# Optimization experiments

Hardware: AMD Instinct MI355X
Metric: run time of the kernel (lower is better)

Reference implementation:

```python
import jax, jax.numpy as jnp
import numpy as np

B, S, I, H = 32, 512, 512, 512


def _complex_tanh(r, i):
    mag = jnp.maximum(jnp.sqrt(r * r + i * i + 1e-14), 1e-8)
    t = jnp.tanh(mag)
    return t * (r / mag), t * (i / mag)


def setup_inputs() -> dict:
    key = jax.random.key(0)
    ks = jax.random.split(key, 32)
    stdv = 1.0 / np.sqrt(H)
    def u(k, shape):
        return jax.random.uniform(k, shape, jnp.float32, -stdv, stdv)
    inp = {
        "z_real": jax.random.normal(ks[0], (B, S, I), jnp.float32),
        "z_imag": jax.random.normal(ks[1], (B, S, I), jnp.float32),
    }
    idx = 2
    for g in ["i", "f", "c", "o"]:
        inp[f"W_z{g}_real"] = u(ks[idx], (I, H)); idx += 1
        inp[f"W_z{g}_imag"] = u(ks[idx], (I, H)); idx += 1
        inp[f"W_h{g}_real"] = u(ks[idx], (H, H)); idx += 1
        inp[f"W_h{g}_imag"] = u(ks[idx], (H, H)); idx += 1
        inp[f"b_{g}_real"] = u(ks[idx], (H,)); idx += 1
        inp[f"b_{g}_imag"] = u(ks[idx], (H,)); idx += 1
    return inp


def reference(z_real, z_imag,
              W_zi_real, W_zi_imag, W_hi_real, W_hi_imag, b_i_real, b_i_imag,
              W_zf_real, W_zf_imag, W_hf_real, W_hf_imag, b_f_real, b_f_imag,
              W_zc_real, W_zc_imag, W_hc_real, W_hc_imag, b_c_real, b_c_imag,
              W_zo_real, W_zo_imag, W_ho_real, W_ho_imag, b_o_real, b_o_imag):
    # Precompute input-side contributions for all timesteps in one batched GEMM each.
    def xproj(Wr, Wi, br):  # real part of z @ (Wr + j Wi), plus real bias
        return (jnp.einsum('bsi,ih->bsh', z_real, Wr)
                - jnp.einsum('bsi,ih->bsh', z_imag, Wi) + br)
    xi = xproj(W_zi_real, W_zi_imag, b_i_real)
    xf = xproj(W_zf_real, W_zf_imag, b_f_real)
    xo = xproj(W_zo_real, W_zo_imag, b_o_real)
    xc_r = xproj(W_zc_real, W_zc_imag, b_c_real)
    xc_i = (jnp.einsum('bsi,ih->bsh', z_imag, W_zc_real)
            + jnp.einsum('bsi,ih->bsh', z_real, W_zc_imag) + b_c_imag)

    bsz = z_real.shape[0]
    hdim = W_hi_real.shape[0]
    init = (jnp.zeros((bsz, hdim), z_real.dtype),) * 4  # h_r, h_i, c_r, c_i

    def step(carry, x):
        h_r, h_i, c_r, c_i = carry
        xi_t, xf_t, xo_t, xcr_t, xci_t = x
        i_t = jax.nn.sigmoid(xi_t + h_r @ W_hi_real - h_i @ W_hi_imag)
        f_t = jax.nn.sigmoid(xf_t + h_r @ W_hf_real - h_i @ W_hf_imag)
        o_t = jax.nn.sigmoid(xo_t + h_r @ W_ho_real - h_i @ W_ho_imag)
        ct_r = xcr_t + h_r @ W_hc_real - h_i @ W_hc_imag
        ct_i = xci_t + h_i @ W_hc_real + h_r @ W_hc_imag
        ct_r, ct_i = _complex_tanh(ct_r, ct_i)
        c_r = f_t * c_r + i_t * ct_r
        c_i = f_t * c_i + i_t * ct_i
        th_r, th_i = _complex_tanh(c_r, c_i)
        h_r = o_t * th_r
        h_i = o_t * th_i
        return (h_r, h_i, c_r, c_i), (h_r, h_i)

    xs = tuple(a.transpose(1, 0, 2) for a in (xi, xf, xo, xc_r, xc_i))  # (S,B,H)
    (hf_r, hf_i, cf_r, cf_i), (seq_r, seq_i) = jax.lax.scan(step, init, xs)
    hseq_r = seq_r.transpose(1, 0, 2)  # (B,S,H)
    hseq_i = seq_i.transpose(1, 0, 2)
    return ((hseq_r, hseq_i), ((hf_r, hf_i), (cf_r, cf_i)))
```

## Files before the change

kernel.cpp:

```cpp
#include <hip/hip_runtime.h>

#define OFF_WZT   0ull
#define OFF_WHT   5242880ull
#define OFF_BIAS  10485760ull
#define OFF_XPERM 10496000ull
#define OFF_HBUF  94382080ull
#define NWG 256

typedef __attribute__((ext_vector_type(8))) short short8;
typedef __attribute__((ext_vector_type(4))) float f32x4;

__device__ __forceinline__ unsigned short f2bf(float f) {
  unsigned int u = __float_as_uint(f);
  u += 0x7fffu + ((u >> 16) & 1u);
  return (unsigned short)(u >> 16);
}
__device__ __forceinline__ float bf2f(unsigned short h) {
  return __uint_as_float(((unsigned int)h) << 16);
}

struct PackArgs {
  const float* zlo[5]; const float* zhi[5];
  const float* hlo[5]; const float* hhi[5];
  const float* bias[5];
};

__global__ void pack_kernel(PackArgs args, unsigned short* __restrict__ WzT,
                            unsigned short* __restrict__ WhT,
                            float* __restrict__ bias_out,
                            unsigned long long* __restrict__ Hbuf64) {
  const long long total = 2ll * 2621440ll;
  long long stride = (long long)gridDim.x * blockDim.x;
  for (long long gid = (long long)blockIdx.x * blockDim.x + threadIdx.x; gid < total; gid += stride) {
    int sel = (int)(gid >= 2621440ll);
    int e = (int)(gid - (long long)sel * 2621440ll);
    int c = e >> 10, k = e & 1023;
    int g = c >> 9, h = c & 511;
    float v;
    if (sel) {
      int kk = k >> 1, ri = k & 1;
      const float* src = ri ? args.hhi[g] : args.hlo[g];
      float sgn = (!ri || g == 4) ? 1.f : -1.f;
      v = sgn * src[kk * 512 + h];
    } else {
      int kk = k & 511;
      const float* src = (k < 512) ? args.zlo[g] : args.zhi[g];
      float sgn = (k < 512 || g == 4) ? 1.f : -1.f;
      v = sgn * src[kk * 512 + h];
    }
    (sel ? WhT : WzT)[(long long)c * 1024 + k] = f2bf(v);
  }
  int gid0 = blockIdx.x * blockDim.x + threadIdx.x;
  if (gid0 < 2560) { int g = gid0 >> 9; bias_out[gid0] = args.bias[g][gid0 & 511]; }
  if (gid0 < 32768) Hbuf64[gid0] = 0ull;
}

__global__ __launch_bounds__(256) void phase1_kernel(
    const float* __restrict__ zr, const float* __restrict__ zi,
    const unsigned short* __restrict__ WzT, const float* __restrict__ bias,
    unsigned short* __restrict__ Xperm) {
  __shared__ unsigned short Al[64 * 40];
  __shared__ unsigned short Bl[64 * 40];
  int bid = blockIdx.x;
  int bm = bid / 40, bn = bid % 40;
  int tid = threadIdx.x;
  int wave = tid >> 6, lane = tid & 63;
  int mq = wave >> 1, nq = wave & 1;
  int lr = lane & 15, lkb = (lane >> 4) * 8;
  int srow = tid >> 2, sq = tid & 3;

  f32x4 acc[2][2];
#pragma unroll
  for (int i0 = 0; i0 < 2; i0++)
#pragma unroll
    for (int j0 = 0; j0 < 2; j0++) acc[i0][j0] = (f32x4){0.f, 0.f, 0.f, 0.f};

  for (int kb = 0; kb < 32; kb++) {
    int gk = kb * 32 + sq * 8;
    const float* srcp = (gk < 512) ? (zr + (long long)(bm * 64 + srow) * 512 + gk)
                                   : (zi + (long long)(bm * 64 + srow) * 512 + (gk - 512));
    float4 f0 = *(const float4*)srcp;
    float4 f1 = *(const float4*)(srcp + 4);
    uint4 p;
    p.x = (unsigned)f2bf(f0.x) | ((unsigned)f2bf(f0.y) << 16);
    p.y = (unsigned)f2bf(f0.z) | ((unsigned)f2bf(f0.w) << 16);
    p.z = (unsigned)f2bf(f1.x) | ((unsigned)f2bf(f1.y) << 16);
    p.w = (unsigned)f2bf(f1.z) | ((unsigned)f2bf(f1.w) << 16);
    *(uint4*)(&Al[srow * 40 + sq * 8]) = p;
    const unsigned short* bsrc = WzT + (long long)(bn * 64 + srow) * 1024 + kb * 32 + sq * 8;
    *(uint4*)(&Bl[srow * 40 + sq * 8]) = *(const uint4*)bsrc;
    __syncthreads();
    short8 a0 = *(const short8*)(&Al[(mq * 32 + 0 + lr) * 40 + lkb]);
    short8 a1 = *(const short8*)(&Al[(mq * 32 + 16 + lr) * 40 + lkb]);
    short8 b0 = *(const short8*)(&Bl[(nq * 32 + 0 + lr) * 40 + lkb]);
    short8 b1 = *(const short8*)(&Bl[(nq * 32 + 16 + lr) * 40 + lkb]);
    acc[0][0] = __builtin_amdgcn_mfma_f32_16x16x32_bf16(a0, b0, acc[0][0], 0, 0, 0);
    acc[0][1] = __builtin_amdgcn_mfma_f32_16x16x32_bf16(a0, b1, acc[0][1], 0, 0, 0);
    acc[1][0] = __builtin_amdgcn_mfma_f32_16x16x32_bf16(a1, b0, acc[1][0], 0, 0, 0);
    acc[1][1] = __builtin_amdgcn_mfma_f32_16x16x32_bf16(a1, b1, acc[1][1], 0, 0, 0);
    __syncthreads();
  }
#pragma unroll
  for (int mt = 0; mt < 2; mt++)
#pragma unroll
    for (int nt = 0; nt < 2; nt++) {
      int C = bn * 64 + nq * 32 + nt * 16 + lr;
      float bv = bias[C];
      int g = C >> 9, h = C & 511;
      int wgc = h >> 3, jj = h & 7;
#pragma unroll
      for (int r = 0; r < 4; r++) {
        int R = bm * 64 + mq * 32 + mt * 16 + (lane >> 4) * 4 + r;
        int bb = R >> 9, tt = R & 511;
        float v = acc[mt][nt][r] + bv;
        Xperm[(((long long)(tt * 64 + wgc)) * 32 + bb) * 40 + g * 8 + jj] = f2bf(v);
      }
    }
}

__global__ __launch_bounds__(384) void recur_kernel(
    const unsigned short* __restrict__ WhT,
    const unsigned short* __restrict__ Xperm,
    unsigned long long* __restrict__ Hbuf64,
    float* __restrict__ out) {
  extern __shared__ unsigned short lds[];
  unsigned short* Wl = lds;
  unsigned int* Hl32 = (unsigned int*)(lds + 41280);
  float* gates = (float*)((char*)(lds + 41280) + 32768);

  int bid = blockIdx.x;
  int d = bid >> 6, wl = bid & 63;
  int tid = threadIdx.x;
  int wave = tid >> 6, lane = tid & 63;
  int nt = wave % 3, kh = wave / 3;
  int lr = lane & 15, kq = lane >> 4;

  for (int idx = tid; idx < 5120; idx += 384) {
    int r = idx >> 7, ch = idx & 127;
    int gcol = (r >> 3) * 512 + wl * 8 + (r & 7);
    uint4 v = *(const uint4*)(WhT + (long long)gcol * 1024 + ch * 8);
    *(uint4*)(&Wl[r * 1032 + ch * 8]) = v;
  }
  {
    uint4 z = {0u, 0u, 0u, 0u};
    for (int idx = tid; idx < 2048; idx += 384) ((uint4*)Hl32)[idx] = z;
  }
  __syncthreads();

  unsigned long long* Hme = Hbuf64 + d * 8192;
  const int nch = (tid < 256) ? 11 : 10;
  const unsigned need = (tid < 256) ? 0x7FFu : 0x3FFu;

  float c_r = 0.f, c_i = 0.f;
  int er = tid >> 3, ej = tid & 7;

  for (int t = 0; t < 512; t++) {
    float xg[5];
    if (tid < 64) {
      const unsigned short* xp = Xperm + (((long long)(t * 64 + wl)) * 32 + (8 * d + er)) * 40;
#pragma unroll
      for (int g = 0; g < 5; g++) xg[g] = bf2f(xp[g * 8 + ej]);
    }

    if (t > 0) {
      const unsigned long long* hb = Hme + ((t - 1) & 1) * 4096;
      unsigned long long v[11];
      unsigned got = 0;
      while (true) {
#pragma unroll
        for (int p = 0; p < 11; p++) {
          if (p < nch && !(got & (1u << p)))
            v[p] = __hip_atomic_load(hb + tid + p * 384, __ATOMIC_RELAXED,
                                     __HIP_MEMORY_SCOPE_AGENT);
        }
        unsigned g2 = got;
#pragma unroll
        for (int p = 0; p < 11; p++)
          if (p < nch && !(got & (1u << p)) && (unsigned)(v[p] >> 32) == (unsigned)t)
            g2 |= 1u << p;
        got = g2;
        if (got == need) break;
        __builtin_amdgcn_s_sleep(1);
      }
#pragma unroll
      for (int p = 0; p < 11; p++)
        if (p < nch) {
          int c = tid + p * 384;
          Hl32[((c >> 5) * 16 + ((c >> 2) & 7)) * 4 + (c & 3)] = (unsigned)v[p];
        }
    }
    __syncthreads();

    f32x4 acc0 = {0.f, 0.f, 0.f, 0.f};
    f32x4 acc1 = {0.f, 0.f, 0.f, 0.f};
    const unsigned short* Hls = (const unsigned short*)Hl32;
#pragma unroll
    for (int kk = 0; kk < 8; kk++) {
      int ka = kh * 16 + kk;
      short8 a = *(const short8*)(Hls + (ka * 4 + kq) * 128 + lr * 8);
      short8 b = *(const short8*)(&Wl[(nt * 16 + lr) * 1032 + ka * 32 + kq * 8]);
      acc0 = __builtin_amdgcn_mfma_f32_16x16x32_bf16(a, b, acc0, 0, 0, 0);
    }
#pragma unroll
    for (int kk = 8; kk < 16; kk++) {
      int ka = kh * 16 + kk;
      short8 a = *(const short8*)(Hls + (ka * 4 + kq) * 128 + lr * 8);
      short8 b = *(const short8*)(&Wl[(nt * 16 + lr) * 1032 + ka * 32 + kq * 8]);
      acc1 = __builtin_amdgcn_mfma_f32_16x16x32_bf16(a, b, acc1, 0, 0, 0);
    }
    {
      int r0 = (lane >> 4) * 4;
#pragma unroll
      for (int r = 0; r < 4; r++)
        gates[wave * 256 + (r0 + r) * 16 + lr] = acc0[r] + acc1[r];
    }
    __syncthreads();

    if (tid < 64) {
      float gv[5];
#pragma unroll
      for (int g = 0; g < 5; g++) {
        int c = g * 8 + ej, tn = c >> 4, cw = c & 15;
        gv[g] = gates[tn * 256 + er * 16 + cw] + gates[(3 + tn) * 256 + er * 16 + cw] + xg[g];
      }
      float ig = 1.f / (1.f + __expf(-gv[0]));
      float fg = 1.f / (1.f + __expf(-gv[1]));
      float og = 1.f / (1.f + __expf(-gv[2]));
      float crp = gv[3], cip = gv[4];
      float mag = fmaxf(sqrtf(crp * crp + cip * cip + 1e-14f), 1e-8f);
      float e1 = __expf(-2.f * mag);
      float s1 = ((1.f - e1) / (1.f + e1)) / mag;
      c_r = fg * c_r + ig * (crp * s1);
      c_i = fg * c_i + ig * (cip * s1);
      float mag2 = fmaxf(sqrtf(c_r * c_r + c_i * c_i + 1e-14f), 1e-8f);
      float e2 = __expf(-2.f * mag2);
      float s2 = ((1.f - e2) / (1.f + e2)) / mag2;
      float hr = og * (c_r * s2);
      float hi = og * (c_i * s2);
      int j = wl * 8 + ej;
      int cidx = ((j >> 2) * 8 + er) * 4 + (j & 3);
      unsigned hv = (unsigned)f2bf(hr) | ((unsigned)f2bf(hi) << 16);
      __hip_atomic_store(Hme + (t & 1) * 4096 + cidx,
                         ((unsigned long long)(t + 1) << 32) | hv,
                         __ATOMIC_RELAXED, __HIP_MEMORY_SCOPE_AGENT);
      int b = 8 * d + er;
      out[(long long)b * 262144 + t * 512 + j] = hr;
      out[8388608ll + (long long)b * 262144 + t * 512 + j] = hi;
      if (t == 511) {
        out[16777216ll + b * 512 + j] = hr;
        out[16793600ll + b * 512 + j] = hi;
        out[16809984ll + b * 512 + j] = c_r;
        out[16826368ll + b * 512 + j] = c_i;
      }
    }
  }
}

extern "C" void kernel_launch(void* const* d_in, const int* in_sizes, int n_in,
                              void* d_out, int out_size, void* d_ws, size_t ws_size,
                              hipStream_t stream) {
  const float* zr = (const float*)d_in[0];
  const float* zi = (const float*)d_in[1];
  const int gi = 2, gf = 8, gc = 14, go = 20;
  PackArgs pa;
  const int gbase[5] = {gi, gf, go, gc, gc};
  for (int g = 0; g < 5; g++) {
    int b = gbase[g];
    if (g < 4) {
      pa.zlo[g] = (const float*)d_in[b + 0];
      pa.zhi[g] = (const float*)d_in[b + 1];
      pa.hlo[g] = (const float*)d_in[b + 2];
      pa.hhi[g] = (const float*)d_in[b + 3];
    } else {
      pa.zlo[g] = (const float*)d_in[b + 1];
      pa.zhi[g] = (const float*)d_in[b + 0];
      pa.hlo[g] = (const float*)d_in[b + 3];
      pa.hhi[g] = (const float*)d_in[b + 2];
    }
  }
  pa.bias[0] = (const float*)d_in[gi + 4];
  pa.bias[1] = (const float*)d_in[gf + 4];
  pa.bias[2] = (const float*)d_in[go + 4];
  pa.bias[3] = (const float*)d_in[gc + 4];
  pa.bias[4] = (const float*)d_in[gc + 5];

  char* ws = (char*)d_ws;
  unsigned short* WzT = (unsigned short*)(ws + OFF_WZT);
  unsigned short* WhT = (unsigned short*)(ws + OFF_WHT);
  float* bias = (float*)(ws + OFF_BIAS);
  unsigned short* Xperm = (unsigned short*)(ws + OFF_XPERM);
  unsigned long long* Hbuf64 = (unsigned long long*)(ws + OFF_HBUF);

  pack_kernel<<<2048, 256, 0, stream>>>(pa, WzT, WhT, bias, Hbuf64);
  phase1_kernel<<<10240, 256, 0, stream>>>(zr, zi, WzT, bias, Xperm);

  const int ldsBytes = 82560 + 32768 + 6144;
  (void)hipFuncSetAttribute((const void*)recur_kernel,
                            hipFuncAttributeMaxDynamicSharedMemorySize, ldsBytes);
  recur_kernel<<<NWG, 384, ldsBytes, stream>>>(WhT, Xperm, Hbuf64, (float*)d_out);
}
```

Before: 1.771 ms.

## Keep recurrent weight fragments in registers and offload polling from gate waves

Each wave now loads its 16 B-operand fragments of the recurrent weights into registers once, staged through a reused LDS buffer in two halves. This removes the per-step LDS reads of the weights and cuts LDS use to about 41 KB. Polling for the previous step's hidden state is moved off the first wave, which computes gates, onto the other 320 threads, so the gate wave does not spin. The tanh divisions become reciprocal multiplies. In exchange the kernel holds many more VGPRs, and the remaining waves poll more entries each.

```diff
diff --git a/kernel.cpp b/kernel.cpp
--- a/kernel.cpp
+++ b/kernel.cpp
@@ -124,9 +124,9 @@
     unsigned long long* __restrict__ Hbuf64,
     float* __restrict__ out) {
   extern __shared__ unsigned short lds[];
-  unsigned short* Wl = lds;
-  unsigned int* Hl32 = (unsigned int*)(lds + 41280);
-  float* gates = (float*)((char*)(lds + 41280) + 32768);
+  unsigned short* Wlh = lds;
+  unsigned int* Hl32 = (unsigned int*)lds;
+  float* gates = (float*)((char*)lds + 32768);
 
   int bid = blockIdx.x;
   int d = bid >> 6, wl = bid & 63;
@@ -135,21 +135,39 @@
   int nt = wave % 3, kh = wave / 3;
   int lr = lane & 15, kq = lane >> 4;
 
-  for (int idx = tid; idx < 5120; idx += 384) {
-    int r = idx >> 7, ch = idx & 127;
-    int gcol = (r >> 3) * 512 + wl * 8 + (r & 7);
-    uint4 v = *(const uint4*)(WhT + (long long)gcol * 1024 + ch * 8);
-    *(uint4*)(&Wl[r * 1032 + ch * 8]) = v;
+  short8 breg[16];
+  for (int h = 0; h < 2; h++) {
+#pragma unroll
+    for (int it = 0; it < 7; it++) {
+      int idx = tid + it * 384;
+      if (idx < 2560) {
+        int r = idx >> 6, k8 = idx & 63;
+        int gcol = (r >> 3) * 512 + wl * 8 + (r & 7);
+        *(uint4*)(&Wlh[r * 520 + k8 * 8]) =
+            *(const uint4*)(WhT + (long long)gcol * 1024 + h * 512 + k8 * 8);
+      }
+    }
+    __syncthreads();
+    if (kh == h) {
+#pragma unroll
+      for (int kk = 0; kk < 16; kk++)
+        breg[kk] = *(const short8*)(&Wlh[(nt * 16 + lr) * 520 + kk * 32 + kq * 8]);
+    }
+    __syncthreads();
   }
   {
     uint4 z = {0u, 0u, 0u, 0u};
-    for (int idx = tid; idx < 2048; idx += 384) ((uint4*)Hl32)[idx] = z;
-  }
-  __syncthreads();
+#pragma unroll
+    for (int it = 0; it < 6; it++) {
+      int idx = tid + it * 384;
+      if (idx < 2048) ((uint4*)Hl32)[idx] = z;
+    }
+  }
 
   unsigned long long* Hme = Hbuf64 + d * 8192;
-  const int nch = (tid < 256) ? 11 : 10;
-  const unsigned need = (tid < 256) ? 0x7FFu : 0x3FFu;
+  int pt = tid - 64;
+  const int nch = (pt < 0) ? 0 : (pt < 256 ? 13 : 12);
+  const unsigned need = (pt < 0) ? 0u : (pt < 256 ? 0x1FFFu : 0xFFFu);
 
   float c_r = 0.f, c_i = 0.f;
   int er = tid >> 3, ej = tid & 7;
@@ -162,20 +180,19 @@
       for (int g = 0; g < 5; g++) xg[g] = bf2f(xp[g * 8 + ej]);
     }
 
-    if (t > 0) {
+    if (t > 0 && tid >= 64) {
       const unsigned long long* hb = Hme + ((t - 1) & 1) * 4096;
-      unsigned long long v[11];
+      unsigned long long v[13];
       unsigned got = 0;
       while (true) {
 #pragma unroll
-        for (int p = 0; p < 11; p++) {
+        for (int p = 0; p < 13; p++)
           if (p < nch && !(got & (1u << p)))
-            v[p] = __hip_atomic_load(hb + tid + p * 384, __ATOMIC_RELAXED,
+            v[p] = __hip_atomic_load(hb + pt + p * 320, __ATOMIC_RELAXED,
                                      __HIP_MEMORY_SCOPE_AGENT);
-        }
         unsigned g2 = got;
 #pragma unroll
-        for (int p = 0; p < 11; p++)
+        for (int p = 0; p < 13; p++)
           if (p < nch && !(got & (1u << p)) && (unsigned)(v[p] >> 32) == (unsigned)t)
             g2 |= 1u << p;
         got = g2;
@@ -183,9 +200,9 @@
         __builtin_amdgcn_s_sleep(1);
       }
 #pragma unroll
-      for (int p = 0; p < 11; p++)
+      for (int p = 0; p < 13; p++)
         if (p < nch) {
-          int c = tid + p * 384;
+          int c = pt + p * 320;
           Hl32[((c >> 5) * 16 + ((c >> 2) & 7)) * 4 + (c & 3)] = (unsigned)v[p];
         }
     }
@@ -198,15 +215,13 @@
     for (int kk = 0; kk < 8; kk++) {
       int ka = kh * 16 + kk;
       short8 a = *(const short8*)(Hls + (ka * 4 + kq) * 128 + lr * 8);
-      short8 b = *(const short8*)(&Wl[(nt * 16 + lr) * 1032 + ka * 32 + kq * 8]);
-      acc0 = __builtin_amdgcn_mfma_f32_16x16x32_bf16(a, b, acc0, 0, 0, 0);
+      acc0 = __builtin_amdgcn_mfma_f32_16x16x32_bf16(a, breg[kk], acc0, 0, 0, 0);
     }
 #pragma unroll
     for (int kk = 8; kk < 16; kk++) {
       int ka = kh * 16 + kk;
       short8 a = *(const short8*)(Hls + (ka * 4 + kq) * 128 + lr * 8);
-      short8 b = *(const short8*)(&Wl[(nt * 16 + lr) * 1032 + ka * 32 + kq * 8]);
-      acc1 = __builtin_amdgcn_mfma_f32_16x16x32_bf16(a, b, acc1, 0, 0, 0);
+      acc1 = __builtin_amdgcn_mfma_f32_16x16x32_bf16(a, breg[kk], acc1, 0, 0, 0);
     }
     {
       int r0 = (lane >> 4) * 4;
@@ -229,12 +244,12 @@
       float crp = gv[3], cip = gv[4];
       float mag = fmaxf(sqrtf(crp * crp + cip * cip + 1e-14f), 1e-8f);
       float e1 = __expf(-2.f * mag);
-      float s1 = ((1.f - e1) / (1.f + e1)) / mag;
+      float s1 = (1.f - e1) * __frcp_rn((1.f + e1) * mag);
       c_r = fg * c_r + ig * (crp * s1);
       c_i = fg * c_i + ig * (cip * s1);
       float mag2 = fmaxf(sqrtf(c_r * c_r + c_i * c_i + 1e-14f), 1e-8f);
       float e2 = __expf(-2.f * mag2);
-      float s2 = ((1.f - e2) / (1.f + e2)) / mag2;
+      float s2 = (1.f - e2) * __frcp_rn((1.f + e2) * mag2);
       float hr = og * (c_r * s2);
       float hi = og * (c_i * s2);
       int j = wl * 8 + ej;
@@ -294,7 +309,7 @@
   pack_kernel<<<2048, 256, 0, stream>>>(pa, WzT, WhT, bias, Hbuf64);
   phase1_kernel<<<10240, 256, 0, stream>>>(zr, zi, WzT, bias, Xperm);
 
-  const int ldsBytes = 82560 + 32768 + 6144;
+  const int ldsBytes = 41600;
   (void)hipFuncSetAttribute((const void*)recur_kernel,
                             hipFuncAttributeMaxDynamicSharedMemorySize, ldsBytes);
   recur_kernel<<<NWG, 384, ldsBytes, stream>>>(WhT, Xperm, Hbuf64, (float*)d_out);
```

New measurement: 1.797 ms. Within noise of the previous version (+1.4%).

## Hold recurrent weights in registers and split polling and compute waves

Applied to the files above, without the earlier changes.

The recurrent kernel now keeps each compute wave's slice of the hidden-to-hidden weights in registers, so the per-step weight reads from LDS go away. Four waves run the MFMA loop and the gate math, while four separate waves poll the global h buffer and scatter h into LDS. This leaves one barrier per timestep instead of two. The input-projection layout is reordered so each lane reads its five gate values contiguously, and the tanh divides are replaced with a reciprocal. The risk is high register pressure from 32 short8 weight registers under launch bounds of (512, 2), which could cause spills.

```diff
diff --git a/kernel.cpp b/kernel.cpp
--- a/kernel.cpp
+++ b/kernel.cpp
@@ -113,145 +113,137 @@
         int R = bm * 64 + mq * 32 + mt * 16 + (lane >> 4) * 4 + r;
         int bb = R >> 9, tt = R & 511;
         float v = acc[mt][nt][r] + bv;
-        Xperm[(((long long)(tt * 64 + wgc)) * 32 + bb) * 40 + g * 8 + jj] = f2bf(v);
-      }
-    }
-}
-
-__global__ __launch_bounds__(384) void recur_kernel(
+        Xperm[(((long long)(tt * 64 + wgc)) * 32 + bb) * 40 + jj * 5 + g] = f2bf(v);
+      }
+    }
+}
+
+__global__ __launch_bounds__(512, 2) void recur_kernel(
     const unsigned short* __restrict__ WhT,
     const unsigned short* __restrict__ Xperm,
     unsigned long long* __restrict__ Hbuf64,
     float* __restrict__ out) {
-  extern __shared__ unsigned short lds[];
-  unsigned short* Wl = lds;
-  unsigned int* Hl32 = (unsigned int*)(lds + 41280);
-  float* gates = (float*)((char*)(lds + 41280) + 32768);
+  extern __shared__ char ldsraw[];
+  unsigned int* Hl32 = (unsigned int*)ldsraw;
+  float* gatesLds = (float*)(ldsraw + 32768);
 
   int bid = blockIdx.x;
   int d = bid >> 6, wl = bid & 63;
   int tid = threadIdx.x;
   int wave = tid >> 6, lane = tid & 63;
-  int nt = wave % 3, kh = wave / 3;
   int lr = lane & 15, kq = lane >> 4;
-
-  for (int idx = tid; idx < 5120; idx += 384) {
-    int r = idx >> 7, ch = idx & 127;
-    int gcol = (r >> 3) * 512 + wl * 8 + (r & 7);
-    uint4 v = *(const uint4*)(WhT + (long long)gcol * 1024 + ch * 8);
-    *(uint4*)(&Wl[r * 1032 + ch * 8]) = v;
+  int nt = wave;
+
+  short8 breg[32];
+  if (wave < 4) {
+    int g = lr % 5;
+    int hj2 = (lr >= 5) ? 1 : 0;
+    int gcol = g * 512 + wl * 8 + nt * 2 + hj2;
+    const unsigned short* wsrc = WhT + (long long)gcol * 1024 + kq * 8;
+#pragma unroll
+    for (int kk = 0; kk < 32; kk++)
+      breg[kk] = *(const short8*)(wsrc + kk * 32);
   }
   {
     uint4 z = {0u, 0u, 0u, 0u};
-    for (int idx = tid; idx < 2048; idx += 384) ((uint4*)Hl32)[idx] = z;
-  }
-  __syncthreads();
+#pragma unroll
+    for (int i = 0; i < 4; i++) ((uint4*)Hl32)[tid + i * 512] = z;
+  }
 
   unsigned long long* Hme = Hbuf64 + d * 8192;
-  const int nch = (tid < 256) ? 11 : 10;
-  const unsigned need = (tid < 256) ? 0x7FFu : 0x3FFu;
-
   float c_r = 0.f, c_i = 0.f;
-  int er = tid >> 3, ej = tid & 7;
+  int hj = lane >> 3, r = lane & 7;
+  int pt = tid - 256;
 
   for (int t = 0; t < 512; t++) {
-    float xg[5];
-    if (tid < 64) {
-      const unsigned short* xp = Xperm + (((long long)(t * 64 + wl)) * 32 + (8 * d + er)) * 40;
-#pragma unroll
-      for (int g = 0; g < 5; g++) xg[g] = bf2f(xp[g * 8 + ej]);
-    }
-
-    if (t > 0) {
-      const unsigned long long* hb = Hme + ((t - 1) & 1) * 4096;
-      unsigned long long v[11];
-      unsigned got = 0;
-      while (true) {
-#pragma unroll
-        for (int p = 0; p < 11; p++) {
-          if (p < nch && !(got & (1u << p)))
-            v[p] = __hip_atomic_load(hb + tid + p * 384, __ATOMIC_RELAXED,
-                                     __HIP_MEMORY_SCOPE_AGENT);
+    if (wave < 4) {
+      float xg[5];
+      if (lane < 16) {
+        const unsigned short* xp =
+            Xperm + (((long long)(t * 64 + wl)) * 32 + (8 * d + r)) * 40 + (nt * 2 + hj) * 5;
+#pragma unroll
+        for (int g = 0; g < 5; g++) xg[g] = bf2f(xp[g]);
+      }
+      __syncthreads();
+
+      f32x4 acc[4];
+#pragma unroll
+      for (int q = 0; q < 4; q++) acc[q] = (f32x4){0.f, 0.f, 0.f, 0.f};
+      const unsigned short* Hls = (const unsigned short*)Hl32;
+#pragma unroll
+      for (int kk = 0; kk < 32; kk++) {
+        short8 a = *(const short8*)(Hls + (kk * 4 + kq) * 128 + lr * 8);
+        acc[kk & 3] = __builtin_amdgcn_mfma_f32_16x16x32_bf16(a, breg[kk], acc[kk & 3], 0, 0, 0);
+      }
+      f32x4 as = (acc[0] + acc[1]) + (acc[2] + acc[3]);
+
+      float* gb = gatesLds + wave * 256;
+#pragma unroll
+      for (int q = 0; q < 4; q++) gb[q * 64 + lane] = as[q];
+
+      if (lane < 16) {
+        int q = lane & 3, s = (lane & 7) >> 2;
+        float gv[5];
+#pragma unroll
+        for (int g = 0; g < 5; g++)
+          gv[g] = gb[q * 64 + (hj * 5 + g + 16 * s)] + xg[g];
+        float ig = 1.f / (1.f + __expf(-gv[0]));
+        float fg = 1.f / (1.f + __expf(-gv[1]));
+        float og = 1.f / (1.f + __expf(-gv[2]));
+        float crp = gv[3], cip = gv[4];
+        float mag = fmaxf(sqrtf(crp * crp + cip * cip + 1e-14f), 1e-8f);
+        float e1 = __expf(-2.f * mag);
+        float s1 = (1.f - e1) * __frcp_rn((1.f + e1) * mag);
+        c_r = fg * c_r + ig * (crp * s1);
+        c_i = fg * c_i + ig * (cip * s1);
+        float mag2 = fmaxf(sqrtf(c_r * c_r + c_i * c_i + 1e-14f), 1e-8f);
+        float e2 = __expf(-2.f * mag2);
+        float s2 = (1.f - e2) * __frcp_rn((1.f + e2) * mag2);
+        float hr = og * (c_r * s2);
+        float hi = og * (c_i * s2);
+        int j = wl * 8 + nt * 2 + hj;
+        int cidx = ((j >> 2) * 8 + r) * 4 + (j & 3);
+        unsigned hv = (unsigned)f2bf(hr) | ((unsigned)f2bf(hi) << 16);
+        __hip_atomic_store(Hme + (t & 1) * 4096 + cidx,
+                           ((unsigned long long)(t + 1) << 32) | hv,
+                           __ATOMIC_RELAXED, __HIP_MEMORY_SCOPE_AGENT);
+        int b = 8 * d + r;
+        out[(long long)b * 262144 + t * 512 + j] = hr;
+        out[8388608ll + (long long)b * 262144 + t * 512 + j] = hi;
+        if (t == 511) {
+          out[16777216ll + b * 512 + j] = hr;
+          out[16793600ll + b * 512 + j] = hi;
+          out[16809984ll + b * 512 + j] = c_r;
+          out[16826368ll + b * 512 + j] = c_i;
         }
-        unsigned g2 = got;
-#pragma unroll
-        for (int p = 0; p < 11; p++)
-          if (p < nch && !(got & (1u << p)) && (unsigned)(v[p] >> 32) == (unsigned)t)
-            g2 |= 1u << p;
-        got = g2;
-        if (got == need) break;
-        __builtin_amdgcn_s_sleep(1);
-      }
-#pragma unroll
-      for (int p = 0; p < 11; p++)
-        if (p < nch) {
-          int c = tid + p * 384;
+      }
+    } else {
+      if (t > 0) {
+        const unsigned long long* hb = Hme + ((t - 1) & 1) * 4096;
+        unsigned long long v[16];
+        unsigned got = 0;
+        while (true) {
+#pragma unroll
+          for (int p = 0; p < 16; p++)
+            if (!(got & (1u << p)))
+              v[p] = __hip_atomic_load(hb + pt + p * 256, __ATOMIC_RELAXED,
+                                       __HIP_MEMORY_SCOPE_AGENT);
+          unsigned g2 = got;
+#pragma unroll
+          for (int p = 0; p < 16; p++)
+            if (!(got & (1u << p)) && (unsigned)(v[p] >> 32) == (unsigned)t)
+              g2 |= 1u << p;
+          got = g2;
+          if (got == 0xFFFFu) break;
+          __builtin_amdgcn_s_sleep(1);
+        }
+#pragma unroll
+        for (int p = 0; p < 16; p++) {
+          int c = pt + p * 256;
           Hl32[((c >> 5) * 16 + ((c >> 2) & 7)) * 4 + (c & 3)] = (unsigned)v[p];
         }
-    }
-    __syncthreads();
-
-    f32x4 acc0 = {0.f, 0.f, 0.f, 0.f};
-    f32x4 acc1 = {0.f, 0.f, 0.f, 0.f};
-    const unsigned short* Hls = (const unsigned short*)Hl32;
-#pragma unroll
-    for (int kk = 0; kk < 8; kk++) {
-      int ka = kh * 16 + kk;
-      short8 a = *(const short8*)(Hls + (ka * 4 + kq) * 128 + lr * 8);
-      short8 b = *(const short8*)(&Wl[(nt * 16 + lr) * 1032 + ka * 32 + kq * 8]);
-      acc0 = __builtin_amdgcn_mfma_f32_16x16x32_bf16(a, b, acc0, 0, 0, 0);
-    }
-#pragma unroll
-    for (int kk = 8; kk < 16; kk++) {
-      int ka = kh * 16 + kk;
-      short8 a = *(const short8*)(Hls + (ka * 4 + kq) * 128 + lr * 8);
-      short8 b = *(const short8*)(&Wl[(nt * 16 + lr) * 1032 + ka * 32 + kq * 8]);
-      acc1 = __builtin_amdgcn_mfma_f32_16x16x32_bf16(a, b, acc1, 0, 0, 0);
-    }
-    {
-      int r0 = (lane >> 4) * 4;
-#pragma unroll
-      for (int r = 0; r < 4; r++)
-        gates[wave * 256 + (r0 + r) * 16 + lr] = acc0[r] + acc1[r];
-    }
-    __syncthreads();
-
-    if (tid < 64) {
-      float gv[5];
-#pragma unroll
-      for (int g = 0; g < 5; g++) {
-        int c = g * 8 + ej, tn = c >> 4, cw = c & 15;
-        gv[g] = gates[tn * 256 + er * 16 + cw] + gates[(3 + tn) * 256 + er * 16 + cw] + xg[g];
-      }
-      float ig = 1.f / (1.f + __expf(-gv[0]));
-      float fg = 1.f / (1.f + __expf(-gv[1]));
-      float og = 1.f / (1.f + __expf(-gv[2]));
-      float crp = gv[3], cip = gv[4];
-      float mag = fmaxf(sqrtf(crp * crp + cip * cip + 1e-14f), 1e-8f);
-      float e1 = __expf(-2.f * mag);
-      float s1 = ((1.f - e1) / (1.f + e1)) / mag;
-      c_r = fg * c_r + ig * (crp * s1);
-      c_i = fg * c_i + ig * (cip * s1);
-      float mag2 = fmaxf(sqrtf(c_r * c_r + c_i * c_i + 1e-14f), 1e-8f);
-      float e2 = __expf(-2.f * mag2);
-      float s2 = ((1.f - e2) / (1.f + e2)) / mag2;
-      float hr = og * (c_r * s2);
-      float hi = og * (c_i * s2);
-      int j = wl * 8 + ej;
-      int cidx = ((j >> 2) * 8 + er) * 4 + (j & 3);
-      unsigned hv = (unsigned)f2bf(hr) | ((unsigned)f2bf(hi) << 16);
-      __hip_atomic_store(Hme + (t & 1) * 4096 + cidx,
-                         ((unsigned long long)(t + 1) << 32) | hv,
-                         __ATOMIC_RELAXED, __HIP_MEMORY_SCOPE_AGENT);
-      int b = 8 * d + er;
-      out[(long long)b * 262144 + t * 512 + j] = hr;
-      out[8388608ll + (long long)b * 262144 + t * 512 + j] = hi;
-      if (t == 511) {
-        out[16777216ll + b * 512 + j] = hr;
-        out[16793600ll + b * 512 + j] = hi;
-        out[16809984ll + b * 512 + j] = c_r;
-        out[16826368ll + b * 512 + j] = c_i;
-      }
+      }
+      __syncthreads();
     }
   }
 }
@@ -294,8 +286,8 @@
   pack_kernel<<<2048, 256, 0, stream>>>(pa, WzT, WhT, bias, Hbuf64);
   phase1_kernel<<<10240, 256, 0, stream>>>(zr, zi, WzT, bias, Xperm);
 
-  const int ldsBytes = 82560 + 32768 + 6144;
+  const int ldsBytes = 81920;
   (void)hipFuncSetAttribute((const void*)recur_kernel,
                             hipFuncAttributeMaxDynamicSharedMemorySize, ldsBytes);
-  recur_kernel<<<NWG, 384, ldsBytes, stream>>>(WhT, Xperm, Hbuf64, (float*)d_out);
-}
+  recur_kernel<<<NWG, 512, ldsBytes, stream>>>(WhT, Xperm, Hbuf64, (float*)d_out);
+}
```

Result: slower. 2.001 ms (+13.0%).

## Split recurrence across 512 workgroups with register-resident weights and sentinel sync

Applied to the files above, without the earlier changes.

The recurrent kernel now runs 512 workgroups, each handling 4 batch rows instead of 8, so the per-step cross-workgroup exchange per group is smaller. The recurrent weight slice moves from LDS into registers, and LDS shrinks to a small H buffer plus the gate scratch. Each workgroup spins on a per-group sentinel array before reading the tagged H values. The design depends on all 512 workgroups being co-resident for the spin barrier, and it wastes MFMA lanes because only 4 of the 16 A rows are used.

```diff
diff --git a/kernel.cpp b/kernel.cpp
--- a/kernel.cpp
+++ b/kernel.cpp
@@ -5,7 +5,8 @@
 #define OFF_BIAS  10485760ull
 #define OFF_XPERM 10496000ull
 #define OFF_HBUF  94382080ull
-#define NWG 256
+#define OFF_SENT  94644224ull
+#define NWG 512
 
 typedef __attribute__((ext_vector_type(8))) short short8;
 typedef __attribute__((ext_vector_type(4))) float f32x4;
@@ -28,7 +29,8 @@
 __global__ void pack_kernel(PackArgs args, unsigned short* __restrict__ WzT,
                             unsigned short* __restrict__ WhT,
                             float* __restrict__ bias_out,
-                            unsigned long long* __restrict__ Hbuf64) {
+                            unsigned long long* __restrict__ Hbuf64,
+                            unsigned int* __restrict__ Sent) {
   const long long total = 2ll * 2621440ll;
   long long stride = (long long)gridDim.x * blockDim.x;
   for (long long gid = (long long)blockIdx.x * blockDim.x + threadIdx.x; gid < total; gid += stride) {
@@ -53,6 +55,7 @@
   int gid0 = blockIdx.x * blockDim.x + threadIdx.x;
   if (gid0 < 2560) { int g = gid0 >> 9; bias_out[gid0] = args.bias[g][gid0 & 511]; }
   if (gid0 < 32768) Hbuf64[gid0] = 0ull;
+  if (gid0 < 512) Sent[gid0] = 0u;
 }
 
 __global__ __launch_bounds__(256) void phase1_kernel(
@@ -118,15 +121,14 @@
     }
 }
 
-__global__ __launch_bounds__(384) void recur_kernel(
+__global__ __launch_bounds__(384, 3) void recur_kernel(
     const unsigned short* __restrict__ WhT,
     const unsigned short* __restrict__ Xperm,
     unsigned long long* __restrict__ Hbuf64,
+    unsigned int* __restrict__ Sent,
     float* __restrict__ out) {
-  extern __shared__ unsigned short lds[];
-  unsigned short* Wl = lds;
-  unsigned int* Hl32 = (unsigned int*)(lds + 41280);
-  float* gates = (float*)((char*)(lds + 41280) + 32768);
+  __shared__ unsigned int Hl32[2048 + 16];
+  __shared__ float gates[1536];
 
   int bid = blockIdx.x;
   int d = bid >> 6, wl = bid & 63;
@@ -135,122 +137,132 @@
   int nt = wave % 3, kh = wave / 3;
   int lr = lane & 15, kq = lane >> 4;
 
-  for (int idx = tid; idx < 5120; idx += 384) {
-    int r = idx >> 7, ch = idx & 127;
-    int gcol = (r >> 3) * 512 + wl * 8 + (r & 7);
-    uint4 v = *(const uint4*)(WhT + (long long)gcol * 1024 + ch * 8);
-    *(uint4*)(&Wl[r * 1032 + ch * 8]) = v;
-  }
+  short8 breg[16];
   {
-    uint4 z = {0u, 0u, 0u, 0u};
-    for (int idx = tid; idx < 2048; idx += 384) ((uint4*)Hl32)[idx] = z;
-  }
+    int c = nt * 16 + lr; if (c > 39) c = 39;
+    int g = c >> 3, jj = c & 7;
+    int gcol = g * 512 + wl * 8 + jj;
+    const unsigned short* wsrc = WhT + (long long)gcol * 1024 + kh * 512 + kq * 8;
+#pragma unroll
+    for (int kk = 0; kk < 16; kk++)
+      breg[kk] = *(const short8*)(wsrc + kk * 32);
+  }
+  for (int i = tid; i < 2064; i += 384) Hl32[i] = 0u;
   __syncthreads();
 
-  unsigned long long* Hme = Hbuf64 + d * 8192;
-  const int nch = (tid < 256) ? 11 : 10;
-  const unsigned need = (tid < 256) ? 0x7FFu : 0x3FFu;
-
+  unsigned long long* Hme = Hbuf64 + d * 4096;
+  unsigned int* Sme = Sent + d * 64;
   float c_r = 0.f, c_i = 0.f;
-  int er = tid >> 3, ej = tid & 7;
+  int er = lane >> 3, ej = lane & 7;
+  int np = (tid < 128) ? 6 : 5;
 
   for (int t = 0; t < 512; t++) {
     float xg[5];
-    if (tid < 64) {
-      const unsigned short* xp = Xperm + (((long long)(t * 64 + wl)) * 32 + (8 * d + er)) * 40;
+    if (wave == 0 && lane < 32) {
+      const unsigned short* xp =
+          Xperm + (((long long)(t * 64 + wl)) * 32 + (4 * d + er)) * 40;
 #pragma unroll
       for (int g = 0; g < 5; g++) xg[g] = bf2f(xp[g * 8 + ej]);
     }
 
     if (t > 0) {
-      const unsigned long long* hb = Hme + ((t - 1) & 1) * 4096;
-      unsigned long long v[11];
-      unsigned got = 0;
       while (true) {
-#pragma unroll
-        for (int p = 0; p < 11; p++) {
-          if (p < nch && !(got & (1u << p)))
+        unsigned sv = __hip_atomic_load(Sme + lane, __ATOMIC_RELAXED,
+                                        __HIP_MEMORY_SCOPE_AGENT);
+        if (__all(sv >= (unsigned)t)) break;
+        __builtin_amdgcn_s_sleep(1);
+      }
+      const unsigned long long* hb = Hme + ((t - 1) & 1) * 2048;
+      unsigned long long v[6];
+#pragma unroll
+      for (int p = 0; p < 6; p++)
+        if (p < np)
+          v[p] = __hip_atomic_load(hb + tid + p * 384, __ATOMIC_RELAXED,
+                                   __HIP_MEMORY_SCOPE_AGENT);
+#pragma unroll
+      for (int p = 0; p < 6; p++)
+        if (p < np) {
+          while ((unsigned)(v[p] >> 32) != (unsigned)t)
             v[p] = __hip_atomic_load(hb + tid + p * 384, __ATOMIC_RELAXED,
                                      __HIP_MEMORY_SCOPE_AGENT);
-        }
-        unsigned g2 = got;
-#pragma unroll
-        for (int p = 0; p < 11; p++)
-          if (p < nch && !(got & (1u << p)) && (unsigned)(v[p] >> 32) == (unsigned)t)
-            g2 |= 1u << p;
-        got = g2;
-        if (got == need) break;
-        __builtin_amdgcn_s_sleep(1);
-      }
-#pragma unroll
-      for (int p = 0; p < 11; p++)
-        if (p < nch) {
-          int c = tid + p * 384;
-          Hl32[((c >> 5) * 16 + ((c >> 2) & 7)) * 4 + (c & 3)] = (unsigned)v[p];
+          Hl32[tid + p * 384] = (unsigned)v[p];
         }
     }
     __syncthreads();
 
     f32x4 acc0 = {0.f, 0.f, 0.f, 0.f};
     f32x4 acc1 = {0.f, 0.f, 0.f, 0.f};
-    const unsigned short* Hls = (const unsigned short*)Hl32;
 #pragma unroll
     for (int kk = 0; kk < 8; kk++) {
       int ka = kh * 16 + kk;
-      short8 a = *(const short8*)(Hls + (ka * 4 + kq) * 128 + lr * 8);
-      short8 b = *(const short8*)(&Wl[(nt * 16 + lr) * 1032 + ka * 32 + kq * 8]);
-      acc0 = __builtin_amdgcn_mfma_f32_16x16x32_bf16(a, b, acc0, 0, 0, 0);
+      const unsigned int* ap = (lr < 4) ? (Hl32 + ((ka * 4 + kq) * 4 + lr) * 4)
+                                        : (Hl32 + 2048);
+      short8 a = *(const short8*)ap;
+      acc0 = __builtin_amdgcn_mfma_f32_16x16x32_bf16(a, breg[kk], acc0, 0, 0, 0);
     }
 #pragma unroll
     for (int kk = 8; kk < 16; kk++) {
       int ka = kh * 16 + kk;
-      short8 a = *(const short8*)(Hls + (ka * 4 + kq) * 128 + lr * 8);
-      short8 b = *(const short8*)(&Wl[(nt * 16 + lr) * 1032 + ka * 32 + kq * 8]);
-      acc1 = __builtin_amdgcn_mfma_f32_16x16x32_bf16(a, b, acc1, 0, 0, 0);
+      const unsigned int* ap = (lr < 4) ? (Hl32 + ((ka * 4 + kq) * 4 + lr) * 4)
+                                        : (Hl32 + 2048);
+      short8 a = *(const short8*)ap;
+      acc1 = __builtin_amdgcn_mfma_f32_16x16x32_bf16(a, breg[kk], acc1, 0, 0, 0);
     }
     {
-      int r0 = (lane >> 4) * 4;
+      f32x4 as = acc0 + acc1;
+      int r0 = kq * 4;
 #pragma unroll
       for (int r = 0; r < 4; r++)
-        gates[wave * 256 + (r0 + r) * 16 + lr] = acc0[r] + acc1[r];
+        gates[wave * 256 + (r0 + r) * 16 + lr] = as[r];
     }
     __syncthreads();
 
-    if (tid < 64) {
-      float gv[5];
-#pragma unroll
-      for (int g = 0; g < 5; g++) {
-        int c = g * 8 + ej, tn = c >> 4, cw = c & 15;
-        gv[g] = gates[tn * 256 + er * 16 + cw] + gates[(3 + tn) * 256 + er * 16 + cw] + xg[g];
+    if (wave == 0) {
+      float hr = 0.f, hi = 0.f;
+      if (lane < 32) {
+        float gv[5];
+#pragma unroll
+        for (int g = 0; g < 5; g++) {
+          int c = g * 8 + ej, tn = c >> 4, cw = c & 15;
+          gv[g] = gates[tn * 256 + er * 16 + cw] +
+                  gates[(3 + tn) * 256 + er * 16 + cw] + xg[g];
+        }
+        float ig = 1.f / (1.f + __expf(-gv[0]));
+        float fg = 1.f / (1.f + __expf(-gv[1]));
+        float og = 1.f / (1.f + __expf(-gv[2]));
+        float crp = gv[3], cip = gv[4];
+        float mag = fmaxf(sqrtf(crp * crp + cip * cip + 1e-14f), 1e-8f);
+        float e1 = __expf(-2.f * mag);
+        float s1 = (1.f - e1) * __frcp_rn((1.f + e1) * mag);
+        c_r = fg * c_r + ig * (crp * s1);
+        c_i = fg * c_i + ig * (cip * s1);
+        float mag2 = fmaxf(sqrtf(c_r * c_r + c_i * c_i + 1e-14f), 1e-8f);
+        float e2 = __expf(-2.f * mag2);
+        float s2 = (1.f - e2) * __frcp_rn((1.f + e2) * mag2);
+        hr = og * (c_r * s2);
+        hi = og * (c_i * s2);
+        int j = wl * 8 + ej;
+        int ci = (j >> 2) * 16 + er * 4 + (j & 3);
+        unsigned hv = (unsigned)f2bf(hr) | ((unsigned)f2bf(hi) << 16);
+        __hip_atomic_store(Hme + (t & 1) * 2048 + ci,
+                           ((unsigned long long)(t + 1) << 32) | hv,
+                           __ATOMIC_RELAXED, __HIP_MEMORY_SCOPE_AGENT);
       }
-      float ig = 1.f / (1.f + __expf(-gv[0]));
-      float fg = 1.f / (1.f + __expf(-gv[1]));
-      float og = 1.f / (1.f + __expf(-gv[2]));
-      float crp = gv[3], cip = gv[4];
-      float mag = fmaxf(sqrtf(crp * crp + cip * cip + 1e-14f), 1e-8f);
-      float e1 = __expf(-2.f * mag);
-      float s1 = ((1.f - e1) / (1.f + e1)) / mag;
-      c_r = fg * c_r + ig * (crp * s1);
-      c_i = fg * c_i + ig * (cip * s1);
-      float mag2 = fmaxf(sqrtf(c_r * c_r + c_i * c_i + 1e-14f), 1e-8f);
-      float e2 = __expf(-2.f * mag2);
-      float s2 = ((1.f - e2) / (1.f + e2)) / mag2;
-      float hr = og * (c_r * s2);
-      float hi = og * (c_i * s2);
-      int j = wl * 8 + ej;
-      int cidx = ((j >> 2) * 8 + er) * 4 + (j & 3);
-      unsigned hv = (unsigned)f2bf(hr) | ((unsigned)f2bf(hi) << 16);
-      __hip_atomic_store(Hme + (t & 1) * 4096 + cidx,
-                         ((unsigned long long)(t + 1) << 32) | hv,
-                         __ATOMIC_RELAXED, __HIP_MEMORY_SCOPE_AGENT);
-      int b = 8 * d + er;
-      out[(long long)b * 262144 + t * 512 + j] = hr;
-      out[8388608ll + (long long)b * 262144 + t * 512 + j] = hi;
-      if (t == 511) {
-        out[16777216ll + b * 512 + j] = hr;
-        out[16793600ll + b * 512 + j] = hi;
-        out[16809984ll + b * 512 + j] = c_r;
-        out[16826368ll + b * 512 + j] = c_i;
+      asm volatile("s_waitcnt vmcnt(0)" ::: "memory");
+      if (lane == 0)
+        __hip_atomic_store(Sme + wl, (unsigned)(t + 1),
+                           __ATOMIC_RELAXED, __HIP_MEMORY_SCOPE_AGENT);
+      if (lane < 32) {
+        int j = wl * 8 + ej;
+        int b = 4 * d + er;
+        out[(long long)b * 262144 + t * 512 + j] = hr;
+        out[8388608ll + (long long)b * 262144 + t * 512 + j] = hi;
+        if (t == 511) {
+          out[16777216ll + b * 512 + j] = hr;
+          out[16793600ll + b * 512 + j] = hi;
+          out[16809984ll + b * 512 + j] = c_r;
+          out[16826368ll + b * 512 + j] = c_i;
+        }
       }
     }
   }
@@ -290,12 +302,9 @@
   float* bias = (float*)(ws + OFF_BIAS);
   unsigned short* Xperm = (unsigned short*)(ws + OFF_XPERM);
   unsigned long long* Hbuf64 = (unsigned long long*)(ws + OFF_HBUF);
-
-  pack_kernel<<<2048, 256, 0, stream>>>(pa, WzT, WhT, bias, Hbuf64);
+  unsigned int* Sent = (unsigned int*)(ws + OFF_SENT);
+
+  pack_kernel<<<2048, 256, 0, stream>>>(pa, WzT, WhT, bias, Hbuf64, Sent);
   phase1_kernel<<<10240, 256, 0, stream>>>(zr, zi, WzT, bias, Xperm);
-
-  const int ldsBytes = 82560 + 32768 + 6144;
-  (void)hipFuncSetAttribute((const void*)recur_kernel,
-                            hipFuncAttributeMaxDynamicSharedMemorySize, ldsBytes);
-  recur_kernel<<<NWG, 384, ldsBytes, stream>>>(WhT, Xperm, Hbuf64, (float*)d_out);
-}
+  recur_kernel<<<NWG, 384, 0, stream>>>(WhT, Xperm, Hbuf64, Sent, (float*)d_out);
+}
```

Result: slower. 5.403 ms (+205.0%).
